# Optimization experiments

Hardware: AMD Instinct MI355X
Metric: run time of the kernel (lower is better)

## Reference

```python
import jax, jax.numpy as jnp
import numpy as np

SHAPES = ((28, 28, 28), (14, 14, 14), (7, 7, 7))  # (D,H,W) per level, hardcoded by offset_normalizer
M, L, P = 6, 3, 4  # n_heads, n_levels, n_points


def grid_sample_3d(vol, grid):
    """Trilinear grid sample, zeros padding, align_corners=False.
    vol: (B, C, D, H, W); grid: (B, Q, 3) with xyz in [-1,1] (x->W, y->H, z->D).
    Returns (B, C, Q)."""
    B, C, D, H, W = vol.shape
    x = ((grid[..., 0] + 1.0) * W - 1.0) * 0.5
    y = ((grid[..., 1] + 1.0) * H - 1.0) * 0.5
    z = ((grid[..., 2] + 1.0) * D - 1.0) * 0.5
    x0f = jnp.floor(x); y0f = jnp.floor(y); z0f = jnp.floor(z)
    fx = x - x0f; fy = y - y0f; fz = z - z0f
    x0 = x0f.astype(jnp.int32); y0 = y0f.astype(jnp.int32); z0 = z0f.astype(jnp.int32)
    flat = vol.reshape(B, C, D * H * W)
    out = jnp.zeros((B, C, grid.shape[1]), vol.dtype)
    for dz, wz in ((0, 1.0 - fz), (1, fz)):
        for dy, wy in ((0, 1.0 - fy), (1, fy)):
            for dx, wx in ((0, 1.0 - fx), (1, fx)):
                zi = z0 + dz; yi = y0 + dy; xi = x0 + dx
                valid = (zi >= 0) & (zi < D) & (yi >= 0) & (yi < H) & (xi >= 0) & (xi < W)
                idx = (jnp.clip(zi, 0, D - 1) * H + jnp.clip(yi, 0, H - 1)) * W + jnp.clip(xi, 0, W - 1)
                g = jnp.take_along_axis(flat, idx[:, None, :], axis=2)  # (B,C,Q)
                w = (wz * wy * wx) * valid.astype(vol.dtype)
                out = out + g * w[:, None, :]
    return out


def setup_inputs() -> dict:
    key = jax.random.key(0)
    ks = jax.random.split(key, 8)
    bs, Lq, d_model, image_dim, T = 1, 4096, 768, 1408, 2
    S = sum(d * h * w for d, h, w in SHAPES)  # 25039
    return {
        "query": jax.random.normal(ks[0], (bs, Lq, d_model), jnp.float32),
        "reference_points": jax.random.uniform(ks[1], (bs, Lq, 3), jnp.float32),
        "value": jax.random.normal(ks[2], (bs, T, S, image_dim), jnp.float32),
        "Wv": jax.random.normal(ks[3], (image_dim, d_model), jnp.float32) * 0.02,
        "bv": jnp.zeros((d_model,), jnp.float32),
        "Woff": jax.random.normal(ks[4], (d_model, M * T * L * P * 3), jnp.float32) * 0.02,
        "boff": jax.random.normal(ks[5], (M * T * L * P * 3,), jnp.float32) * 0.5,
        "Wa": jax.random.normal(ks[6], (d_model, M * T * L * P), jnp.float32) * 0.02,
        "ba": jnp.zeros((M * T * L * P,), jnp.float32),
        "Wo": jax.random.normal(ks[7], (d_model, d_model), jnp.float32) * 0.02,
        "bo": jnp.zeros((d_model,), jnp.float32),
    }


def reference(query, reference_points, value, Wv, bv, Woff, boff, Wa, ba, Wo, bo):
    N, Lq, d_model = query.shape
    T = value.shape[1]
    Dh = d_model // M
    # value projection + head split: (N,T,S,M,Dh)
    v = (value @ Wv + bv).reshape(N, T, -1, M, Dh)
    # sampling offsets and attention weights from query
    off = (query @ Woff + boff).reshape(N, Lq, M, T, L, P, 3)
    aw = jax.nn.softmax((query @ Wa + ba).reshape(N, Lq, M, T * L * P), axis=-1)
    aw = aw.reshape(N, Lq, M, T, L, P)
    normalizer = jnp.asarray([[28., 28., 28.], [14., 14., 14.], [7., 7., 7.]], query.dtype)
    loc = reference_points[:, :, None, None, None, None, :] + off / normalizer[None, None, None, None, :, None, :]
    grids = 2.0 * loc - 1.0  # (N,Lq,M,T,L,P,3)
    starts = [0]
    for (d, h, w) in SHAPES:
        starts.append(starts[-1] + d * h * w)
    sampled = []
    for l, (Dl, Hl, Wl) in enumerate(SHAPES):
        vl = v[:, :, starts[l]:starts[l + 1]]                       # (N,T,Sl,M,Dh)
        vl = vl.transpose(0, 1, 3, 4, 2).reshape(N * T * M, Dh, Dl, Hl, Wl)
        gl = grids[:, :, :, :, l].transpose(0, 3, 2, 1, 4, 5).reshape(N * T * M, Lq * P, 3)
        sampled.append(grid_sample_3d(vl, gl).reshape(N, T, M, Dh, Lq, P))
    s = jnp.stack(sampled, axis=5)                                  # (N,T,M,Dh,Lq,L,P)
    out = jnp.einsum('ntmdqlp,nqmtlp->nqmd', s, aw).reshape(N, Lq, M * Dh)
    return out @ Wo + bo
```

## Files before the change

kernel.cpp:

```cpp
#include <hip/hip_runtime.h>
#include <hip/hip_bf16.h>
#include <stdint.h>

#define LQ    4096
#define DMOD  768
#define IMGD  1408
#define TT    2
#define MM    6
#define LL    3
#define PP    4
#define DH    128
#define STOT  25039
#define OFFC  432
#define AWC   144
#define PROJC 576
#define NSAMP 24
#define NCORN 192

typedef __attribute__((ext_vector_type(8))) __bf16 bf16x8;
typedef __attribute__((ext_vector_type(4))) float  f32x4;

__device__ __forceinline__ void gl_lds16(const void* g, void* l) {
    __builtin_amdgcn_global_load_lds(
        (const __attribute__((address_space(1))) void*)g,
        (__attribute__((address_space(3))) void*)l, 16, 0, 0);
}

__global__ __launch_bounds__(256) void cvt_transpose(
    const float* __restrict__ W, __bf16* __restrict__ WT, int K, int N)
{
    __shared__ float tile[32][33];
    const int k0 = blockIdx.x * 32, n0 = blockIdx.y * 32;
    const int c = threadIdx.x & 31, r8 = threadIdx.x >> 5;
    #pragma unroll
    for (int i = 0; i < 4; ++i) {
        int r = r8 + i * 8;
        int k = k0 + r, n = n0 + c;
        tile[r][c] = (k < K && n < N) ? W[(size_t)k * N + n] : 0.f;
    }
    __syncthreads();
    #pragma unroll
    for (int i = 0; i < 4; ++i) {
        int r = r8 + i * 8;
        int n = n0 + r, k = k0 + c;
        if (n < N && k < K) WT[(size_t)n * K + k] = (__bf16)tile[c][r];
    }
}

__global__ void concat_bias(const float* __restrict__ boff,
                            const float* __restrict__ ba,
                            float* __restrict__ bcat)
{
    int i = blockIdx.x * blockDim.x + threadIdx.x;
    if (i < PROJC) bcat[i] = (i < OFFC) ? boff[i] : ba[i - OFFC];
}

__global__ __launch_bounds__(256) void cvt_bf16_kernel(
    const float* __restrict__ in, __bf16* __restrict__ out, int n8)
{
    const int stride = gridDim.x * blockDim.x;
    for (int i = blockIdx.x * blockDim.x + threadIdx.x; i < n8; i += stride) {
        const float4* p = (const float4*)(in + (size_t)i * 8);
        float4 v0 = p[0], v1 = p[1];
        bf16x8 o;
        o[0] = (__bf16)v0.x; o[1] = (__bf16)v0.y;
        o[2] = (__bf16)v0.z; o[3] = (__bf16)v0.w;
        o[4] = (__bf16)v1.x; o[5] = (__bf16)v1.y;
        o[6] = (__bf16)v1.z; o[7] = (__bf16)v1.w;
        *(bf16x8*)(out + (size_t)i * 8) = o;
    }
}

__global__ __launch_bounds__(256) void reduce_ksplit(
    const float* __restrict__ parts, const float* __restrict__ bias,
    float* __restrict__ outp, int N, int total)
{
    const size_t stride = (size_t)gridDim.x * blockDim.x * 4;
    for (size_t e = ((size_t)blockIdx.x * blockDim.x + threadIdx.x) * 4;
         e < (size_t)total; e += stride) {
        float4 s0 = *(const float4*)(parts + e);
        float4 s1 = *(const float4*)(parts + e + (size_t)total);
        float4 s2 = *(const float4*)(parts + e + 2 * (size_t)total);
        float4 s3 = *(const float4*)(parts + e + 3 * (size_t)total);
        const int col = (int)(e % (size_t)N);
        float4 r;
        r.x = s0.x + s1.x + s2.x + s3.x + bias[col + 0];
        r.y = s0.y + s1.y + s2.y + s3.y + bias[col + 1];
        r.z = s0.z + s1.z + s2.z + s3.z + bias[col + 2];
        r.w = s0.w + s1.w + s2.w + s3.w + bias[col + 3];
        *(float4*)(outp + e) = r;
    }
}

template<int AF32, int OUT_BF16, int SWZ, int SPLITK = 1>
__global__ __launch_bounds__(256, 3) void gemm_mfma(
    const void* __restrict__ Ap, const __bf16* __restrict__ BT,
    const float* __restrict__ bias, void* __restrict__ Cp,
    int M, int N, int K)
{
    __shared__ __bf16 As[2][128][32];
    __shared__ __bf16 Bs[2][128][32];

    const int tid  = threadIdx.x;
    const int lane = tid & 63;
    const int wave = tid >> 6;
    const int wm = (wave & 1) * 64;
    const int wn = (wave >> 1) * 64;

    int bx, by;
    if constexpr (SWZ > 0) {
        const int bid = blockIdx.x;
        const int xcd = bid & 7;
        const int slot = bid >> 3;
        const int ppx = (gridDim.x >> 3) / SWZ;
        const int pix = slot / SWZ;
        bx = slot - pix * SWZ;
        by = xcd * ppx + pix;
    } else {
        bx = blockIdx.x; by = blockIdx.y;
    }
    const int row0 = by * 128;
    const int col0 = bx * 128;

    const int kLen = (SPLITK > 1) ? (K / SPLITK) : K;
    const int k0   = (SPLITK > 1) ? ((int)blockIdx.z * kLen) : 0;
    float* Cpart = (float*)Cp;
    if constexpr (SPLITK > 1) Cpart += (size_t)blockIdx.z * ((size_t)M * N);

    const int fr = lane & 15;
    const int kq = lane >> 4;

    const int sr  = tid >> 1;
    const int kk0 = (tid & 1) * 16;

    float f[16];

    auto stageB = [&](int ki, int buf) {
        #pragma unroll
        for (int j = 0; j < 2; ++j) {
            const int g   = wave * 128 + j * 64 + lane;
            const int row = g >> 2, cir = g & 3;
            const __bf16* src = BT + (size_t)(col0 + row) * K + k0 + ki * 32 + cir * 8;
            gl_lds16(src, (char*)&Bs[buf][0][0] + (size_t)(wave * 128 + j * 64) * 16);
        }
    };
    auto stageA_lds = [&](int ki, int buf) {
        const __bf16* A = (const __bf16*)Ap;
        #pragma unroll
        for (int j = 0; j < 2; ++j) {
            const int g   = wave * 128 + j * 64 + lane;
            const int row = g >> 2, cir = g & 3;
            const __bf16* src = A + (size_t)(row0 + row) * K + k0 + ki * 32 + cir * 8;
            gl_lds16(src, (char*)&As[buf][0][0] + (size_t)(wave * 128 + j * 64) * 16);
        }
    };
    auto loadA_f32 = [&](int ki) {
        const float* A = (const float*)Ap;
        const int gm = row0 + sr;
        if (gm < M) {
            const float4* ap = (const float4*)(A + (size_t)gm * K + k0 + ki * 32 + kk0);
            #pragma unroll
            for (int i = 0; i < 4; ++i) {
                float4 v = ap[i];
                f[i*4+0] = v.x; f[i*4+1] = v.y; f[i*4+2] = v.z; f[i*4+3] = v.w;
            }
        } else {
            #pragma unroll
            for (int i = 0; i < 16; ++i) f[i] = 0.f;
        }
    };
    auto writeA = [&](int buf) {
        bf16x8 v0, v1;
        #pragma unroll
        for (int i = 0; i < 8; ++i) { v0[i] = (__bf16)f[i]; v1[i] = (__bf16)f[i+8]; }
        *(bf16x8*)&As[buf][sr][kk0]     = v0;
        *(bf16x8*)&As[buf][sr][kk0 + 8] = v1;
    };

    f32x4 acc[4][4] = {};
    const int nk = kLen >> 5;

    stageB(0, 0);
    if constexpr (AF32) { loadA_f32(0); writeA(0); }
    else                { stageA_lds(0, 0); }

    for (int i = 0; i < nk; ++i) {
        __syncthreads();
        const int cur = i & 1, nxt = cur ^ 1;
        const bool more = (i + 1) < nk;

        if (more) {
            stageB(i + 1, nxt);
            if constexpr (AF32) loadA_f32(i + 1);
            else                stageA_lds(i + 1, nxt);
        }

        bf16x8 a[4], b[4];
        #pragma unroll
        for (int mt = 0; mt < 4; ++mt) a[mt] = *(const bf16x8*)&As[cur][wm + mt*16 + fr][kq * 8];
        #pragma unroll
        for (int nt = 0; nt < 4; ++nt) b[nt] = *(const bf16x8*)&Bs[cur][wn + nt*16 + fr][kq * 8];
        #pragma unroll
        for (int mt = 0; mt < 4; ++mt)
            #pragma unroll
            for (int nt = 0; nt < 4; ++nt)
                acc[mt][nt] = __builtin_amdgcn_mfma_f32_16x16x32_bf16(
                    a[mt], b[nt], acc[mt][nt], 0, 0, 0);

        if constexpr (AF32) { if (more) writeA(nxt); }
    }

    const int col = lane & 15;
    const int rq  = (lane >> 4) * 4;
    #pragma unroll
    for (int mt = 0; mt < 4; ++mt) {
        #pragma unroll
        for (int r = 0; r < 4; ++r) {
            const int gm = row0 + wm + mt*16 + rq + r;
            if (gm >= M) continue;
            #pragma unroll
            for (int nt = 0; nt < 4; ++nt) {
                const int gn = col0 + wn + nt*16 + col;
                if (gn < N) {
                    if constexpr (SPLITK > 1) {
                        Cpart[(size_t)gm * N + gn] = acc[mt][nt][r];
                    } else {
                        float v = acc[mt][nt][r] + bias[gn];
                        if constexpr (OUT_BF16)
                            ((__bf16*)Cp)[(size_t)gm * N + gn] = (__bf16)v;
                        else
                            ((float*)Cp)[(size_t)gm * N + gn] = v;
                    }
                }
            }
        }
    }
}

__global__ __launch_bounds__(256) void sample_kernel(
    const float* __restrict__ refp,
    const float* __restrict__ proj,
    const __bf16* __restrict__ vbuf,
    __bf16* __restrict__ attn)
{
    const int wave = threadIdx.x >> 6;
    const int lane = threadIdx.x & 63;
    const int q = blockIdx.x * 4 + wave;
    const int m = blockIdx.y;

    __shared__ float    s_aw[4][NSAMP];
    __shared__ float    s_w[4][NCORN];
    __shared__ uint32_t s_o[4][NCORN];

    if (lane < NSAMP)
        s_aw[wave][lane] = proj[(size_t)q * PROJC + OFFC + m * NSAMP + lane];
    __syncthreads();

    if (lane < NSAMP) {
        float mx = -1e30f;
        #pragma unroll
        for (int i = 0; i < NSAMP; ++i) mx = fmaxf(mx, s_aw[wave][i]);
        float sum = 0.f;
        #pragma unroll
        for (int i = 0; i < NSAMP; ++i) sum += __expf(s_aw[wave][i] - mx);
        const float aww = __expf(s_aw[wave][lane] - mx) / sum;

        const int t = lane / 12;
        const int r = lane - t * 12;
        const int l = r >> 2;
        const int   Dl    = (l == 0) ? 28 : (l == 1) ? 14 : 7;
        const int   start = (l == 0) ? 0  : (l == 1) ? 21952 : 24696;
        const float fD    = (float)Dl;
        const int   base  = t * STOT + start;

        const float* op = proj + (size_t)q * PROJC + m * 72 + lane * 3;
        const float rx = refp[q*3+0], ry = refp[q*3+1], rz = refp[q*3+2];
        float x = rx * fD + op[0] - 0.5f;
        float y = ry * fD + op[1] - 0.5f;
        float z = rz * fD + op[2] - 0.5f;
        float xf = floorf(x), yf = floorf(y), zf = floorf(z);
        float fx = x - xf, fy = y - yf, fz = z - zf;
        int x0 = (int)xf, y0 = (int)yf, z0 = (int)zf;
        float wx[2] = {1.f - fx, fx}, wy[2] = {1.f - fy, fy}, wz[2] = {1.f - fz, fz};
        #pragma unroll
        for (int cc = 0; cc < 8; ++cc) {
            int dx = cc & 1, dy = (cc >> 1) & 1, dz = cc >> 2;
            int xi = x0 + dx, yi = y0 + dy, zi = z0 + dz;
            bool ok = (xi >= 0) & (xi < Dl) & (yi >= 0) & (yi < Dl) &
                      (zi >= 0) & (zi < Dl);
            float    w   = ok ? aww * wx[dx] * wy[dy] * wz[dz] : 0.f;
            uint32_t off = ok ? (uint32_t)(base + (zi * Dl + yi) * Dl + xi) * (768u * 2u) : 0u;
            s_w[wave][lane * 8 + cc] = w;
            s_o[wave][lane * 8 + cc] = off;
        }
    }
    __syncthreads();

    const int h = lane >> 5;
    const int c = lane & 31;
    const char* vb = (const char*)vbuf + ((size_t)m * 128 + c * 4) * 2;
    float a0 = 0.f, a1 = 0.f, a2 = 0.f, a3 = 0.f;
    #pragma unroll 4
    for (int i = 0; i < NCORN / 2; ++i) {
        const float    w   = s_w[wave][2 * i + h];
        const uint32_t off = s_o[wave][2 * i + h];
        const uint2 u = *(const uint2*)(vb + off);
        a0 += w * __uint_as_float(u.x << 16);
        a1 += w * __uint_as_float(u.x & 0xffff0000u);
        a2 += w * __uint_as_float(u.y << 16);
        a3 += w * __uint_as_float(u.y & 0xffff0000u);
    }
    a0 += __shfl_xor(a0, 32);
    a1 += __shfl_xor(a1, 32);
    a2 += __shfl_xor(a2, 32);
    a3 += __shfl_xor(a3, 32);

    if (h == 0) {
        union { __bf16 hh[4]; uint2 u; } pk;
        pk.hh[0] = (__bf16)a0; pk.hh[1] = (__bf16)a1;
        pk.hh[2] = (__bf16)a2; pk.hh[3] = (__bf16)a3;
        *(uint2*)((char*)attn + ((size_t)q * DMOD + m * 128 + c * 4) * 2) = pk.u;
    }
}

extern "C" void kernel_launch(void* const* d_in, const int* in_sizes, int n_in,
                              void* d_out, int out_size, void* d_ws, size_t ws_size,
                              hipStream_t stream) {
    const float* query = (const float*)d_in[0];
    const float* refp  = (const float*)d_in[1];
    const float* value = (const float*)d_in[2];
    const float* Wv    = (const float*)d_in[3];
    const float* bv    = (const float*)d_in[4];
    const float* Woff  = (const float*)d_in[5];
    const float* boff  = (const float*)d_in[6];
    const float* Wa    = (const float*)d_in[7];
    const float* ba    = (const float*)d_in[8];
    const float* Wo    = (const float*)d_in[9];
    const float* bo    = (const float*)d_in[10];
    float* out = (float*)d_out;

    const int    Mv      = TT * STOT;
    const size_t SZ_ABF  = (size_t)Mv * IMGD * 2;
    const size_t SZ_VBUF = (size_t)TT * STOT * DMOD * 2;
    const size_t SZ_PROJ = (size_t)LQ * PROJC * 4;
    const size_t SZ_ATTN = (size_t)LQ * DMOD * 2;
    const size_t SZ_WVT  = (size_t)IMGD * DMOD * 2;
    const size_t SZ_WCAT = (size_t)PROJC * DMOD * 2;
    const size_t SZ_WOT  = (size_t)DMOD * DMOD * 2;
    const size_t SZ_BCAT = (size_t)PROJC * 4;

    const size_t need_cvt = SZ_ABF + SZ_VBUF + SZ_PROJ + SZ_ATTN +
                            SZ_WVT + SZ_WCAT + SZ_WOT + SZ_BCAT;
    const bool use_cvtA = (ws_size >= need_cvt);

    char* p = (char*)d_ws;
    __bf16* abf = nullptr;
    if (use_cvtA) { abf = (__bf16*)p; p += SZ_ABF; }
    __bf16* vbuf  = (__bf16*)p; p += SZ_VBUF;
    float*  proj  = (float*)p;  p += SZ_PROJ;
    __bf16* attn  = (__bf16*)p; p += SZ_ATTN;
    __bf16* wvt   = (__bf16*)p; p += SZ_WVT;
    __bf16* wcatT = (__bf16*)p; p += SZ_WCAT;
    __bf16* woT   = (__bf16*)p; p += SZ_WOT;
    float*  bcat  = (float*)p;

    cvt_transpose<<<dim3((IMGD+31)/32, (DMOD+31)/32), 256, 0, stream>>>(Wv, wvt, IMGD, DMOD);
    cvt_transpose<<<dim3((DMOD+31)/32, (OFFC+31)/32), 256, 0, stream>>>(Woff, wcatT, DMOD, OFFC);
    cvt_transpose<<<dim3((DMOD+31)/32, (AWC +31)/32), 256, 0, stream>>>(Wa, wcatT + (size_t)OFFC * DMOD, DMOD, AWC);
    cvt_transpose<<<dim3((DMOD+31)/32, (DMOD+31)/32), 256, 0, stream>>>(Wo, woT, DMOD, DMOD);
    concat_bias<<<dim3(3), 256, 0, stream>>>(boff, ba, bcat);

    if (use_cvtA) {
        const int n8 = (int)(((size_t)Mv * IMGD) / 8);
        cvt_bf16_kernel<<<dim3(2048), 256, 0, stream>>>(value, abf, n8);
        gemm_mfma<0, 1, 6><<<dim3(2352), 256, 0, stream>>>(
            abf, wvt, bv, vbuf, Mv, DMOD, IMGD);

        float* g2p = (float*)abf;
        gemm_mfma<1, 0, 0, 4><<<dim3(5, 32, 4), 256, 0, stream>>>(
            query, wcatT, nullptr, g2p, LQ, PROJC, DMOD);
        reduce_ksplit<<<dim3(1024), 256, 0, stream>>>(
            g2p, bcat, proj, PROJC, LQ * PROJC);

        sample_kernel<<<dim3(LQ / 4, MM), 256, 0, stream>>>(refp, proj, vbuf, attn);

        float* g3p = (float*)abf;
        gemm_mfma<0, 0, 0, 4><<<dim3(6, 32, 4), 256, 0, stream>>>(
            attn, woT, nullptr, g3p, LQ, DMOD, DMOD);
        reduce_ksplit<<<dim3(1024), 256, 0, stream>>>(
            g3p, bo, out, DMOD, LQ * DMOD);
    } else {
        gemm_mfma<1, 1, 6><<<dim3(2352), 256, 0, stream>>>(
            value, wvt, bv, vbuf, Mv, DMOD, IMGD);
        gemm_mfma<1, 0, 0><<<dim3((PROJC + 127) / 128, LQ / 128), 256, 0, stream>>>(
            query, wcatT, bcat, proj, LQ, PROJC, DMOD);
        sample_kernel<<<dim3(LQ / 4, MM), 256, 0, stream>>>(refp, proj, vbuf, attn);
        gemm_mfma<0, 0, 0><<<dim3(DMOD / 128, LQ / 128), 256, 0, stream>>>(
            attn, woT, bo, out, LQ, DMOD, DMOD);
    }
}
```

Before: 734.8 us.

## Fuse fp32-to-bf16 value conversion into GEMM via direct LDS loads with swizzle

The separate pass that converts the large fp32 value tensor to bf16 is removed. The value-projection GEMM now streams fp32 tiles straight into LDS with global_load_lds and converts to bf16 at fragment-read time. XOR swizzles are added to all A and B LDS layouts to cut bank conflicts. The workspace drops the big bf16 copy and keeps only the split-K partial buffer. The trade-off is doubled LDS for the A tile, which may lower occupancy, plus conversion ALU work inside the main loop.

```diff
diff --git a/kernel.cpp b/kernel.cpp
--- a/kernel.cpp
+++ b/kernel.cpp
@@ -53,22 +53,6 @@
 {
     int i = blockIdx.x * blockDim.x + threadIdx.x;
     if (i < PROJC) bcat[i] = (i < OFFC) ? boff[i] : ba[i - OFFC];
-}
-
-__global__ __launch_bounds__(256) void cvt_bf16_kernel(
-    const float* __restrict__ in, __bf16* __restrict__ out, int n8)
-{
-    const int stride = gridDim.x * blockDim.x;
-    for (int i = blockIdx.x * blockDim.x + threadIdx.x; i < n8; i += stride) {
-        const float4* p = (const float4*)(in + (size_t)i * 8);
-        float4 v0 = p[0], v1 = p[1];
-        bf16x8 o;
-        o[0] = (__bf16)v0.x; o[1] = (__bf16)v0.y;
-        o[2] = (__bf16)v0.z; o[3] = (__bf16)v0.w;
-        o[4] = (__bf16)v1.x; o[5] = (__bf16)v1.y;
-        o[6] = (__bf16)v1.z; o[7] = (__bf16)v1.w;
-        *(bf16x8*)(out + (size_t)i * 8) = o;
-    }
 }
 
 __global__ __launch_bounds__(256) void reduce_ksplit(
@@ -98,8 +82,12 @@
     const float* __restrict__ bias, void* __restrict__ Cp,
     int M, int N, int K)
 {
-    __shared__ __bf16 As[2][128][32];
+    constexpr int ABYTES = (AF32 == 2) ? (2 * 128 * 32 * 4) : (2 * 128 * 32 * 2);
+    __shared__ char   AsRaw[ABYTES];
     __shared__ __bf16 Bs[2][128][32];
+
+    auto AsF = [&](int buf) -> char* { return AsRaw + buf * (128 * 32 * 4); };
+    auto AsB = [&](int buf) -> char* { return AsRaw + buf * (128 * 32 * 2); };
 
     const int tid  = threadIdx.x;
     const int lane = tid & 63;
@@ -140,8 +128,9 @@
         for (int j = 0; j < 2; ++j) {
             const int g   = wave * 128 + j * 64 + lane;
             const int row = g >> 2, cir = g & 3;
-            const __bf16* src = BT + (size_t)(col0 + row) * K + k0 + ki * 32 + cir * 8;
-            gl_lds16(src, (char*)&Bs[buf][0][0] + (size_t)(wave * 128 + j * 64) * 16);
+            const int csw = cir ^ (row & 3);
+            const __bf16* src = BT + (size_t)(col0 + row) * K + k0 + ki * 32 + csw * 8;
+            gl_lds16(src, (char*)&Bs[buf][0][0] + (size_t)g * 16);
         }
     };
     auto stageA_lds = [&](int ki, int buf) {
@@ -150,8 +139,21 @@
         for (int j = 0; j < 2; ++j) {
             const int g   = wave * 128 + j * 64 + lane;
             const int row = g >> 2, cir = g & 3;
-            const __bf16* src = A + (size_t)(row0 + row) * K + k0 + ki * 32 + cir * 8;
-            gl_lds16(src, (char*)&As[buf][0][0] + (size_t)(wave * 128 + j * 64) * 16);
+            const int csw = cir ^ (row & 3);
+            const __bf16* src = A + (size_t)(row0 + row) * K + k0 + ki * 32 + csw * 8;
+            gl_lds16(src, AsB(buf) + (size_t)g * 16);
+        }
+    };
+    auto stageA_f32 = [&](int ki, int buf) {
+        const float* A = (const float*)Ap;
+        #pragma unroll
+        for (int j = 0; j < 4; ++j) {
+            const int g   = j * 256 + wave * 64 + lane;
+            const int row = g >> 3, s = g & 7;
+            const int ssw = s ^ (row & 7);
+            int gm = row0 + row; if (gm >= M) gm = M - 1;
+            const float* src = A + (size_t)gm * K + k0 + ki * 32 + ssw * 4;
+            gl_lds16(src, AsF(buf) + (size_t)g * 16);
         }
     };
     auto loadA_f32 = [&](int ki) {
@@ -173,16 +175,19 @@
         bf16x8 v0, v1;
         #pragma unroll
         for (int i = 0; i < 8; ++i) { v0[i] = (__bf16)f[i]; v1[i] = (__bf16)f[i+8]; }
-        *(bf16x8*)&As[buf][sr][kk0]     = v0;
-        *(bf16x8*)&As[buf][sr][kk0 + 8] = v1;
+        char* base = AsB(buf) + (size_t)sr * 64;
+        const int g0 = kk0 >> 3;
+        *(bf16x8*)(base + (((g0    ) ^ (sr & 3)) << 4)) = v0;
+        *(bf16x8*)(base + (((g0 + 1) ^ (sr & 3)) << 4)) = v1;
     };
 
     f32x4 acc[4][4] = {};
     const int nk = kLen >> 5;
 
     stageB(0, 0);
-    if constexpr (AF32) { loadA_f32(0); writeA(0); }
-    else                { stageA_lds(0, 0); }
+    if constexpr (AF32 == 1)      { loadA_f32(0); writeA(0); }
+    else if constexpr (AF32 == 2) { stageA_f32(0, 0); }
+    else                          { stageA_lds(0, 0); }
 
     for (int i = 0; i < nk; ++i) {
         __syncthreads();
@@ -191,15 +196,36 @@
 
         if (more) {
             stageB(i + 1, nxt);
-            if constexpr (AF32) loadA_f32(i + 1);
-            else                stageA_lds(i + 1, nxt);
+            if constexpr (AF32 == 1)      loadA_f32(i + 1);
+            else if constexpr (AF32 == 2) stageA_f32(i + 1, nxt);
+            else                          stageA_lds(i + 1, nxt);
         }
 
         bf16x8 a[4], b[4];
         #pragma unroll
-        for (int mt = 0; mt < 4; ++mt) a[mt] = *(const bf16x8*)&As[cur][wm + mt*16 + fr][kq * 8];
-        #pragma unroll
-        for (int nt = 0; nt < 4; ++nt) b[nt] = *(const bf16x8*)&Bs[cur][wn + nt*16 + fr][kq * 8];
+        for (int mt = 0; mt < 4; ++mt) {
+            const int row = wm + mt * 16 + fr;
+            if constexpr (AF32 == 2) {
+                const char* rb = AsF(cur) + (size_t)row * 128;
+                f32x4 lo = *(const f32x4*)(rb + ((((kq << 1)    ) ^ (row & 7)) << 4));
+                f32x4 hi = *(const f32x4*)(rb + ((((kq << 1) + 1) ^ (row & 7)) << 4));
+                bf16x8 av;
+                av[0] = (__bf16)lo[0]; av[1] = (__bf16)lo[1];
+                av[2] = (__bf16)lo[2]; av[3] = (__bf16)lo[3];
+                av[4] = (__bf16)hi[0]; av[5] = (__bf16)hi[1];
+                av[6] = (__bf16)hi[2]; av[7] = (__bf16)hi[3];
+                a[mt] = av;
+            } else {
+                const char* rb = AsB(cur) + (size_t)row * 64;
+                a[mt] = *(const bf16x8*)(rb + ((kq ^ (row & 3)) << 4));
+            }
+        }
+        #pragma unroll
+        for (int nt = 0; nt < 4; ++nt) {
+            const int rowb = wn + nt * 16 + fr;
+            b[nt] = *(const bf16x8*)((const char*)&Bs[cur][0][0] +
+                                     (size_t)rowb * 64 + ((kq ^ (rowb & 3)) << 4));
+        }
         #pragma unroll
         for (int mt = 0; mt < 4; ++mt)
             #pragma unroll
@@ -207,7 +233,7 @@
                 acc[mt][nt] = __builtin_amdgcn_mfma_f32_16x16x32_bf16(
                     a[mt], b[nt], acc[mt][nt], 0, 0, 0);
 
-        if constexpr (AF32) { if (more) writeA(nxt); }
+        if constexpr (AF32 == 1) { if (more) writeA(nxt); }
     }
 
     const int col = lane & 15;
@@ -340,7 +366,7 @@
     float* out = (float*)d_out;
 
     const int    Mv      = TT * STOT;
-    const size_t SZ_ABF  = (size_t)Mv * IMGD * 2;
+    const size_t SZ_PART = (size_t)4 * LQ * DMOD * 4;
     const size_t SZ_VBUF = (size_t)TT * STOT * DMOD * 2;
     const size_t SZ_PROJ = (size_t)LQ * PROJC * 4;
     const size_t SZ_ATTN = (size_t)LQ * DMOD * 2;
@@ -349,13 +375,13 @@
     const size_t SZ_WOT  = (size_t)DMOD * DMOD * 2;
     const size_t SZ_BCAT = (size_t)PROJC * 4;
 
-    const size_t need_cvt = SZ_ABF + SZ_VBUF + SZ_PROJ + SZ_ATTN +
-                            SZ_WVT + SZ_WCAT + SZ_WOT + SZ_BCAT;
-    const bool use_cvtA = (ws_size >= need_cvt);
+    const size_t need_split = SZ_PART + SZ_VBUF + SZ_PROJ + SZ_ATTN +
+                              SZ_WVT + SZ_WCAT + SZ_WOT + SZ_BCAT;
+    const bool use_split = (ws_size >= need_split);
 
     char* p = (char*)d_ws;
-    __bf16* abf = nullptr;
-    if (use_cvtA) { abf = (__bf16*)p; p += SZ_ABF; }
+    float* part = nullptr;
+    if (use_split) { part = (float*)p; p += SZ_PART; }
     __bf16* vbuf  = (__bf16*)p; p += SZ_VBUF;
     float*  proj  = (float*)p;  p += SZ_PROJ;
     __bf16* attn  = (__bf16*)p; p += SZ_ATTN;
@@ -370,28 +396,22 @@
     cvt_transpose<<<dim3((DMOD+31)/32, (DMOD+31)/32), 256, 0, stream>>>(Wo, woT, DMOD, DMOD);
     concat_bias<<<dim3(3), 256, 0, stream>>>(boff, ba, bcat);
 
-    if (use_cvtA) {
-        const int n8 = (int)(((size_t)Mv * IMGD) / 8);
-        cvt_bf16_kernel<<<dim3(2048), 256, 0, stream>>>(value, abf, n8);
-        gemm_mfma<0, 1, 6><<<dim3(2352), 256, 0, stream>>>(
-            abf, wvt, bv, vbuf, Mv, DMOD, IMGD);
-
-        float* g2p = (float*)abf;
+    gemm_mfma<2, 1, 6><<<dim3(2352), 256, 0, stream>>>(
+        value, wvt, bv, vbuf, Mv, DMOD, IMGD);
+
+    if (use_split) {
         gemm_mfma<1, 0, 0, 4><<<dim3(5, 32, 4), 256, 0, stream>>>(
-            query, wcatT, nullptr, g2p, LQ, PROJC, DMOD);
+            query, wcatT, nullptr, part, LQ, PROJC, DMOD);
         reduce_ksplit<<<dim3(1024), 256, 0, stream>>>(
-            g2p, bcat, proj, PROJC, LQ * PROJC);
+            part, bcat, proj, PROJC, LQ * PROJC);
 
         sample_kernel<<<dim3(LQ / 4, MM), 256, 0, stream>>>(refp, proj, vbuf, attn);
 
-        float* g3p = (float*)abf;
         gemm_mfma<0, 0, 0, 4><<<dim3(6, 32, 4), 256, 0, stream>>>(
-            attn, woT, nullptr, g3p, LQ, DMOD, DMOD);
+            attn, woT, nullptr, part, LQ, DMOD, DMOD);
         reduce_ksplit<<<dim3(1024), 256, 0, stream>>>(
-            g3p, bo, out, DMOD, LQ * DMOD);
+            part, bo, out, DMOD, LQ * DMOD);
     } else {
-        gemm_mfma<1, 1, 6><<<dim3(2352), 256, 0, stream>>>(
-            value, wvt, bv, vbuf, Mv, DMOD, IMGD);
         gemm_mfma<1, 0, 0><<<dim3((PROJC + 127) / 128, LQ / 128), 256, 0, stream>>>(
             query, wcatT, bcat, proj, LQ, PROJC, DMOD);
         sample_kernel<<<dim3(LQ / 4, MM), 256, 0, stream>>>(refp, proj, vbuf, attn);
```

Result: no change. 738.3 us (+0.5%).
